# Optimization experiments

Measured on AMD Instinct MI355X. Metric: run time of the kernel, lower is better.

The kernel has to match this reference:

```python
import jax, jax.numpy as jnp
import numpy as np

N_NODES = 20000
N_EDGES = 100000
NODE_IN = 16
EDGE_IN = 10
LEAK = 0.1
EPS = 1e-5


def setup_inputs() -> dict:
    key = jax.random.key(0)
    ks = iter(jax.random.split(key, 40))

    def rn(shape, scale):
        return jax.random.normal(next(ks), shape, dtype=jnp.float32) * scale

    inp = {}
    inp["x"] = jax.random.normal(next(ks), (N_NODES, NODE_IN), dtype=jnp.float32)
    inp["e"] = jax.random.normal(next(ks), (N_EDGES, EDGE_IN), dtype=jnp.float32)
    inp["edge_index"] = jax.random.randint(next(ks), (2, N_EDGES), 0, N_NODES, dtype=jnp.int64)
    inp["xbatch"] = jnp.zeros((N_NODES,), dtype=jnp.int64)

    # BatchNorm affine params
    inp["bn_node_g"] = jnp.ones((NODE_IN,), jnp.float32)
    inp["bn_node_b"] = jnp.zeros((NODE_IN,), jnp.float32)
    inp["bn_edge_g"] = jnp.ones((EDGE_IN,), jnp.float32)
    inp["bn_edge_b"] = jnp.zeros((EDGE_IN,), jnp.float32)

    # nn1: Lin(10,16) -> LeakyReLU -> Lin(16, 16*32) -> LeakyReLU
    inp["nn1_w1"] = rn((EDGE_IN, 16), 0.3); inp["nn1_b1"] = jnp.zeros((16,), jnp.float32)
    inp["nn1_w2"] = rn((16, 16 * 32), 0.25); inp["nn1_b2"] = jnp.zeros((16 * 32,), jnp.float32)
    # nn2: Lin(10,32) -> LeakyReLU -> Lin(32, 32*64) -> LeakyReLU
    inp["nn2_w1"] = rn((EDGE_IN, 32), 0.3); inp["nn2_b1"] = jnp.zeros((32,), jnp.float32)
    inp["nn2_w2"] = rn((32, 32 * 64), 0.18); inp["nn2_b2"] = jnp.zeros((32 * 64,), jnp.float32)

    # NNConv root weights + biases
    inp["l1_root"] = rn((16, 32), 0.25); inp["l1_bias"] = jnp.zeros((32,), jnp.float32)
    inp["l2_root"] = rn((32, 64), 0.18); inp["l2_bias"] = jnp.zeros((64,), jnp.float32)

    # edge_pred_mlp: 138 -> 64 -> 32 -> 16 -> 8 -> 2
    dims = [2 * 64 + EDGE_IN, 64, 32, 16, 8, 2]
    for i in range(5):
        inp[f"mlp_w{i+1}"] = rn((dims[i], dims[i + 1]), 1.0 / np.sqrt(dims[i]))
        inp[f"mlp_b{i+1}"] = jnp.zeros((dims[i + 1],), jnp.float32)
    return inp


def _bn(v, g, b):
    # BatchNorm1d, training-mode batch statistics (biased variance), eps=1e-5
    m = v.mean(axis=0)
    var = v.var(axis=0)
    return (v - m) * jax.lax.rsqrt(var + EPS) * g + b


def _lrelu(v):
    return jax.nn.leaky_relu(v, LEAK)


def _nnconv(x, src, dst, e, w1, b1, w2, b2, root, bias, c_in, c_out):
    # edge MLP -> per-edge weight matrix [E, c_in, c_out]
    h = _lrelu(e @ w1 + b1)
    W = _lrelu(h @ w2 + b2).reshape(-1, c_in, c_out)
    # gather source features, per-edge matmul, scatter-add to targets
    msg = jnp.einsum("ei,eio->eo", x[src], W)
    agg = jax.ops.segment_sum(msg, dst, num_segments=x.shape[0])
    return agg + x @ root + bias


def reference(x, e, edge_index, xbatch,
              bn_node_g, bn_node_b, bn_edge_g, bn_edge_b,
              nn1_w1, nn1_b1, nn1_w2, nn1_b2,
              nn2_w1, nn2_b1, nn2_w2, nn2_b2,
              l1_root, l1_bias, l2_root, l2_bias,
              mlp_w1, mlp_b1, mlp_w2, mlp_b2, mlp_w3, mlp_b3,
              mlp_w4, mlp_b4, mlp_w5, mlp_b5):
    src, dst = edge_index[0], edge_index[1]
    e = _bn(e, bn_edge_g, bn_edge_b)
    x = _bn(x, bn_node_g, bn_node_b)
    x = _nnconv(x, src, dst, e, nn1_w1, nn1_b1, nn1_w2, nn1_b2, l1_root, l1_bias, 16, 32)
    x = _nnconv(x, src, dst, e, nn2_w1, nn2_b1, nn2_w2, nn2_b2, l2_root, l2_bias, 32, 64)
    # MetaLayer edge model: cat(source, target, edge_attr) -> MLP -> [E, 2]
    h = jnp.concatenate([x[src], x[dst], e], axis=1)
    h = _lrelu(h @ mlp_w1 + mlp_b1)
    h = _lrelu(h @ mlp_w2 + mlp_b2)
    h = _lrelu(h @ mlp_w3 + mlp_b3)
    h = _lrelu(h @ mlp_w4 + mlp_b4)
    edge_pred = h @ mlp_w5 + mlp_b5
    return edge_pred
```

## Files before the change

### kernel.cpp

```cpp
#include <hip/hip_runtime.h>
#include <cstdint>

#define N_NODES 20000
#define N_EDGES 100000
#define BN_EPS 1e-5f

typedef __attribute__((ext_vector_type(8))) short short8;
typedef __attribute__((ext_vector_type(4))) float floatx4;

__device__ __forceinline__ float lrelu(float v) { return fmaxf(v, 0.1f * v); }
__device__ __forceinline__ float4 ld4(const float* p) { return *reinterpret_cast<const float4*>(p); }
__device__ __forceinline__ float2 ld2(const float* p) { return *reinterpret_cast<const float2*>(p); }

__device__ __forceinline__ void atomAddF(float* p, float v) {
#if defined(__HIP_DEVICE_COMPILE__)
    unsafeAtomicAdd(p, v);
#else
    atomicAdd(p, v);
#endif
}

__device__ __forceinline__ unsigned short f2bf(float f) {
    union { float f; uint32_t u; } v; v.f = f;
    uint32_t r = v.u + 0x7fffu + ((v.u >> 16) & 1u);
    return (unsigned short)(r >> 16);
}
__device__ __forceinline__ uint32_t pack2(float a, float b) {
    return (uint32_t)f2bf(a) | ((uint32_t)f2bf(b) << 16);
}
__device__ __forceinline__ short8 pack8(float4 a, float4 b) {
    union { short8 s; uint32_t u[4]; } r;
    r.u[0] = pack2(a.x, a.y); r.u[1] = pack2(a.z, a.w);
    r.u[2] = pack2(b.x, b.y); r.u[3] = pack2(b.z, b.w);
    return r.s;
}

__device__ void stats10_dev(const float* __restrict__ v, int rows, float* __restrict__ out,
                            int blk, int nblk, float* sh) {
    if (threadIdx.x < 20) sh[threadIdx.x] = 0.f;
    __syncthreads();
    int nf2 = rows * 5;
    int stride = nblk * 256;
    int g = blk * 256 + threadIdx.x;
    int c2 = g % 5;
    float s0 = 0.f, s1 = 0.f, q0 = 0.f, q1 = 0.f;
    const float2* p = reinterpret_cast<const float2*>(v);
    for (int i = g; i < nf2; i += stride) {
        float2 t = p[i];
        s0 += t.x; s1 += t.y; q0 += t.x * t.x; q1 += t.y * t.y;
    }
    atomicAdd(&sh[2 * c2], s0);
    atomicAdd(&sh[2 * c2 + 1], s1);
    atomicAdd(&sh[10 + 2 * c2], q0);
    atomicAdd(&sh[10 + 2 * c2 + 1], q1);
    __syncthreads();
    if (threadIdx.x < 20) atomAddF(&out[threadIdx.x], sh[threadIdx.x]);
}

__device__ void stats16_dev(const float* __restrict__ v, int rows, float* __restrict__ out,
                            int blk, int nblk, float* sh) {
    if (threadIdx.x < 32) sh[threadIdx.x] = 0.f;
    __syncthreads();
    int nf4 = rows * 4;
    int stride = nblk * 256;
    int g = blk * 256 + threadIdx.x;
    int cg = (g & 3) * 4;
    float s[4] = {0.f, 0.f, 0.f, 0.f}, q[4] = {0.f, 0.f, 0.f, 0.f};
    const float4* p = reinterpret_cast<const float4*>(v);
    for (int i = g; i < nf4; i += stride) {
        float4 t = p[i];
        s[0] += t.x; s[1] += t.y; s[2] += t.z; s[3] += t.w;
        q[0] += t.x * t.x; q[1] += t.y * t.y; q[2] += t.z * t.z; q[3] += t.w * t.w;
    }
    #pragma unroll
    for (int off = 32; off >= 4; off >>= 1) {
        #pragma unroll
        for (int j = 0; j < 4; ++j) {
            s[j] += __shfl_down(s[j], off, 64);
            q[j] += __shfl_down(q[j], off, 64);
        }
    }
    if ((threadIdx.x & 63) < 4) {
        #pragma unroll
        for (int j = 0; j < 4; ++j) {
            atomicAdd(&sh[cg + j], s[j]);
            atomicAdd(&sh[16 + cg + j], q[j]);
        }
    }
    __syncthreads();
    if (threadIdx.x < 32) atomAddF(&out[threadIdx.x], sh[threadIdx.x]);
}

template<int CIN, int COUT, int H, int OCH>
__device__ void convpack_row(const float* __restrict__ w2, const float* __restrict__ b2,
                             char* __restrict__ pk, int r) {
    constexpr int NROW = CIN * OCH;
    constexpr int WB = NROW * 64;
    constexpr int PACKB = WB + NROW * 4;
    if (r >= CIN * COUT) return;
    int chunk = r / NROW;
    int rem = r % NROW;
    int i = rem / OCH, ol = rem % OCH;
    int n = i * COUT + chunk * OCH + ol;
    char* base = pk + (size_t)chunk * PACKB;
    uint32_t pkv[16];
    #pragma unroll
    for (int t = 0; t < 16; ++t) pkv[t] = 0;
    #pragma unroll
    for (int k = 0; k < H; k += 2)
        pkv[k >> 1] = pack2(w2[(size_t)k * (CIN * COUT) + n],
                            w2[(size_t)(k + 1) * (CIN * COUT) + n]);
    uint4* ob = reinterpret_cast<uint4*>(base);
    #pragma unroll
    for (int q = 0; q < 4; ++q)
        ob[(size_t)q * NROW + rem] = make_uint4(pkv[4 * q], pkv[4 * q + 1],
                                                pkv[4 * q + 2], pkv[4 * q + 3]);
    ((float*)(base + WB))[rem] = b2[n];
}

#define P1_S10 120
#define P1_S16 120
__global__ __launch_bounds__(256)
void prep1_kernel(const float* __restrict__ e, const float* __restrict__ x,
                  float* __restrict__ stats_e, float* __restrict__ stats_x,
                  const int* __restrict__ dst, int* __restrict__ counts,
                  const float* __restrict__ nn1_w2, const float* __restrict__ nn1_b2, char* __restrict__ cpack1,
                  const float* __restrict__ nn2_w2, const float* __restrict__ nn2_b2, char* __restrict__ cpack2,
                  const float* __restrict__ mw1, unsigned short* __restrict__ w1t,
                  const float* __restrict__ mw2, const float* __restrict__ mb2,
                  const float* __restrict__ mw3, const float* __restrict__ mb3,
                  const float* __restrict__ mw4, const float* __restrict__ mb4,
                  const float* __restrict__ mw5, const float* __restrict__ mb5,
                  float* __restrict__ mlpw)
{
    __shared__ float sh[32];
    int b = blockIdx.x;
    if (b < P1_S10) {
        stats10_dev(e, N_EDGES, stats_e, b, P1_S10, sh);
    } else if (b < P1_S10 + P1_S16) {
        stats16_dev(x, N_NODES, stats_x, b - P1_S10, P1_S16, sh);
    } else if (b < 631) {
        int i = (b - 240) * 256 + threadIdx.x;
        if (i < N_EDGES) atomicAdd(&counts[dst[i]], 1);
    } else if (b < 633) {
        convpack_row<16, 32, 16, 32>(nn1_w2, nn1_b2, cpack1, (b - 631) * 256 + threadIdx.x);
    } else if (b < 641) {
        convpack_row<32, 64, 32, 16>(nn2_w2, nn2_b2, cpack2, (b - 633) * 256 + threadIdx.x);
    } else {
        if (threadIdx.x < 64) {
            int o = threadIdx.x;
            for (int k = 0; k < 160; k += 2) {
                float a = (k < 138) ? mw1[(size_t)k * 64 + o] : 0.f;
                float c = (k + 1 < 138) ? mw1[(size_t)(k + 1) * 64 + o] : 0.f;
                *reinterpret_cast<uint32_t*>(w1t + (size_t)o * 160 + k) = pack2(a, c);
            }
        }
        for (int i = threadIdx.x; i < 2764; i += 256) {
            float v = 0.f;
            if (i < 2048) v = mw2[i];
            else if (i < 2560) v = mw3[i - 2048];
            else if (i < 2688) v = mw4[i - 2560];
            else if (i < 2704) v = mw5[i - 2688];
            else if (i < 2736) v = mb2[i - 2704];
            else if (i < 2752) v = mb3[i - 2736];
            else if (i < 2760) v = mb4[i - 2752];
            else if (i < 2762) v = mb5[i - 2760];
            mlpw[i] = v;
        }
    }
}

__global__ void scan_kernel(const int* __restrict__ counts, int* __restrict__ starts,
                            int* __restrict__ cursor, int n) {
    __shared__ int part[256];
    const int CH = (n + 255) / 256;
    int t = threadIdx.x;
    int lo = t * CH, hi = min(lo + CH, n);
    int s = 0;
    for (int i = lo; i < hi; ++i) s += counts[i];
    part[t] = s;
    __syncthreads();
    if (t == 0) {
        int acc = 0;
        for (int i = 0; i < 256; ++i) { int v = part[i]; part[i] = acc; acc += v; }
    }
    __syncthreads();
    int acc = part[t];
    for (int i = lo; i < hi; ++i) {
        starts[i] = acc; cursor[i] = acc; acc += counts[i];
    }
}

#define P2_N16 1250
#define P2_SCAT 391
#define P2_HGEN 391
__global__ __launch_bounds__(256)
void prep2_kernel(const float* __restrict__ x, const float* __restrict__ stats_x,
                  const float* __restrict__ bn_node_g, const float* __restrict__ bn_node_b,
                  float* __restrict__ x_n,
                  const int* __restrict__ dst, int* __restrict__ cursor, int* __restrict__ elist,
                  const float* __restrict__ e, const float* __restrict__ stats_e,
                  const float* __restrict__ bn_edge_g, const float* __restrict__ bn_edge_b,
                  float* __restrict__ e_n,
                  const float* __restrict__ w1a, const float* __restrict__ b1a,
                  const float* __restrict__ w1b, const float* __restrict__ b1b,
                  unsigned short* __restrict__ h1, unsigned short* __restrict__ h2)
{
    int b = blockIdx.x;
    if (b < P2_N16) {
        int idx = b * 256 + threadIdx.x;
        if (idx >= N_NODES * 16) return;
        int c = idx & 15;
        float N = (float)N_NODES;
        float m = stats_x[c] / N;
        float var = stats_x[16 + c] / N - m * m;
        float sc = rsqrtf(var + BN_EPS) * bn_node_g[c];
        x_n[idx] = (x[idx] - m) * sc + bn_node_b[c];
    } else if (b < P2_N16 + P2_SCAT) {
        int i = (b - P2_N16) * 256 + threadIdx.x;
        if (i < N_EDGES) {
            int p = atomicAdd(&cursor[dst[i]], 1);
            elist[p] = i;
        }
    } else {
        int eg = (b - P2_N16 - P2_SCAT) * 256 + threadIdx.x;
        if (eg >= N_EDGES) return;
        float ev[10];
        float Ecnt = (float)N_EDGES;
        #pragma unroll
        for (int j = 0; j < 10; ++j) {
            float m = stats_e[j] / Ecnt;
            float var = stats_e[10 + j] / Ecnt - m * m;
            float sc = rsqrtf(var + BN_EPS) * bn_edge_g[j];
            ev[j] = (e[(size_t)eg * 10 + j] - m) * sc + bn_edge_b[j];
            e_n[(size_t)eg * 10 + j] = ev[j];
        }
        {
            uint32_t pk[16];
            #pragma unroll
            for (int t = 0; t < 16; ++t) pk[t] = 0;
            #pragma unroll
            for (int k = 0; k < 16; k += 2) {
                float a0 = b1a[k], a1 = b1a[k + 1];
                #pragma unroll
                for (int j = 0; j < 10; ++j) {
                    a0 += ev[j] * w1a[j * 16 + k];
                    a1 += ev[j] * w1a[j * 16 + k + 1];
                }
                pk[k >> 1] = pack2(lrelu(a0), lrelu(a1));
            }
            uint4* o = reinterpret_cast<uint4*>(h1 + (size_t)eg * 32);
            o[0] = make_uint4(pk[0], pk[1], pk[2], pk[3]);
            o[1] = make_uint4(pk[4], pk[5], pk[6], pk[7]);
            o[2] = make_uint4(pk[8], pk[9], pk[10], pk[11]);
            o[3] = make_uint4(pk[12], pk[13], pk[14], pk[15]);
        }
        {
            uint32_t pk[16];
            #pragma unroll
            for (int k = 0; k < 32; k += 2) {
                float a0 = b1b[k], a1 = b1b[k + 1];
                #pragma unroll
                for (int j = 0; j < 10; ++j) {
                    a0 += ev[j] * w1b[j * 32 + k];
                    a1 += ev[j] * w1b[j * 32 + k + 1];
                }
                pk[k >> 1] = pack2(lrelu(a0), lrelu(a1));
            }
            uint4* o = reinterpret_cast<uint4*>(h2 + (size_t)eg * 32);
            o[0] = make_uint4(pk[0], pk[1], pk[2], pk[3]);
            o[1] = make_uint4(pk[4], pk[5], pk[6], pk[7]);
            o[2] = make_uint4(pk[8], pk[9], pk[10], pk[11]);
            o[3] = make_uint4(pk[12], pk[13], pk[14], pk[15]);
        }
    }
}

template<int CIN, int COUT, int OCH, int NE>
__global__ __launch_bounds__(256, 4)
void conv_lds_kernel(const unsigned short* __restrict__ hbuf,
                     const char* __restrict__ pack,
                     const int* __restrict__ src,
                     const float* __restrict__ xin,
                     float* __restrict__ msgbuf,
                     int n_edges)
{
    constexpr int NCH = COUT / OCH;
    constexpr int NROW = CIN * OCH;
    constexpr int WB = NROW * 64;
    constexpr int PACKB = WB + NROW * 4;
    __shared__ char smem[PACKB];

    int tid = threadIdx.x;
    int chunk = blockIdx.x % NCH;
    int eblk = blockIdx.x / NCH;

    {
        const uint4* g = reinterpret_cast<const uint4*>(pack + (size_t)chunk * PACKB);
        uint4* s = reinterpret_cast<uint4*>(smem);
        #pragma unroll 1
        for (int o = tid; o < PACKB / 16; o += 256) s[o] = g[o];
    }
    __syncthreads();

    int wv = tid >> 6, lane = tid & 63;
    int el = lane & 15, quad = lane >> 4;
    int g0 = (eblk * 4 + wv) * NE;

    const unsigned short* wlds = reinterpret_cast<const unsigned short*>(smem)
                                 + ((size_t)quad * NROW + el) * 8;
    const float* blds = reinterpret_cast<const float*>(smem + WB) + quad * 4;

    #pragma unroll 1
    for (int gI = 0; gI < NE; ++gI) {
        int e0 = (g0 + gI) * 16;
        if (e0 >= n_edges) return;
        int e = e0 + el;
        int s = src[e];

        short8 bfrag = *reinterpret_cast<const short8*>(hbuf + (size_t)e * 32 + quad * 8);

        float xr[CIN];
        #pragma unroll
        for (int i = 0; i < CIN; i += 4) {
            float4 v = ld4(xin + (size_t)s * CIN + i);
            xr[i] = v.x; xr[i + 1] = v.y; xr[i + 2] = v.z; xr[i + 3] = v.w;
        }

        floatx4 msg[OCH / 16];
        #pragma unroll
        for (int t = 0; t < OCH / 16; ++t) msg[t] = (floatx4){0.f, 0.f, 0.f, 0.f};

        #pragma unroll 8
        for (int i = 0; i < CIN; ++i) {
            float xi = xr[i];
            #pragma unroll
            for (int ot = 0; ot < OCH / 16; ++ot) {
                short8 af = *reinterpret_cast<const short8*>(wlds + (i * OCH + ot * 16) * 8);
                float4 bb = *reinterpret_cast<const float4*>(blds + i * OCH + ot * 16);
                floatx4 c = {bb.x, bb.y, bb.z, bb.w};
                c = __builtin_amdgcn_mfma_f32_16x16x32_bf16(af, bfrag, c, 0, 0, 0);
                #pragma unroll
                for (int r = 0; r < 4; ++r)
                    msg[ot][r] += xi * lrelu(c[r]);
            }
        }

        float* orow = msgbuf + (size_t)e * COUT + chunk * OCH;
        #pragma unroll
        for (int ot = 0; ot < OCH / 16; ++ot)
            *reinterpret_cast<float4*>(orow + ot * 16 + quad * 4) =
                make_float4(msg[ot][0], msg[ot][1], msg[ot][2], msg[ot][3]);
    }
}

template<int CIN, int C>
__global__ __launch_bounds__(256)
void gather_root_kernel(const float* __restrict__ xin, const float* __restrict__ w,
                        const float* __restrict__ bias,
                        const float* __restrict__ msg,
                        const int* __restrict__ starts, const int* __restrict__ counts,
                        const int* __restrict__ elist,
                        float* __restrict__ xout, int nodes)
{
    constexpr int NPW = 64 / C;
    int wv = blockIdx.x * 4 + (threadIdx.x >> 6);
    int lane = threadIdx.x & 63;
    int node = wv * NPW + lane / C;
    int ch = lane % C;
    if (node >= nodes) return;
    float acc = bias[ch];
    const float* xrow = xin + (size_t)node * CIN;
    #pragma unroll
    for (int i = 0; i < CIN; ++i) acc += xrow[i] * w[i * C + ch];
    int s0 = starts[node], cnt = counts[node];
    int i = 0;
    for (; i + 3 < cnt; i += 4) {
        int ea = elist[s0 + i], eb = elist[s0 + i + 1];
        int ec = elist[s0 + i + 2], ed = elist[s0 + i + 3];
        float m0 = msg[(size_t)ea * C + ch];
        float m1 = msg[(size_t)eb * C + ch];
        float m2 = msg[(size_t)ec * C + ch];
        float m3 = msg[(size_t)ed * C + ch];
        acc += (m0 + m1) + (m2 + m3);
    }
    for (; i < cnt; ++i) acc += msg[(size_t)elist[s0 + i] * C + ch];
    xout[(size_t)node * C + ch] = acc;
}

__global__ __launch_bounds__(256)
void mlp2_kernel(const float* __restrict__ x2, const float* __restrict__ e_n,
                 const int* __restrict__ src, const int* __restrict__ dst,
                 const unsigned short* __restrict__ w1t, const float* __restrict__ b1,
                 const float* __restrict__ mlpw,
                 float* __restrict__ out, int n_edges)
{
    __shared__ float wl[2764];
    __shared__ float a1t[4 * 1092];
    __shared__ float a2scr[4 * 528];

    int tid = threadIdx.x;
    {
        const uint4* g = reinterpret_cast<const uint4*>(mlpw);
        uint4* s = reinterpret_cast<uint4*>(wl);
        #pragma unroll 1
        for (int i = tid; i < 691; i += 256) s[i] = g[i];
    }

    int wv = tid >> 6, lane = tid & 63;
    int el = lane & 15, quad = lane >> 4;
    int e = blockIdx.x * 64 + wv * 16 + el;
    int eS = (e < n_edges) ? e : (n_edges - 1);
    int sN = src[eS], dN = dst[eS];

    short8 bf[5];
    {
        const float* rs = x2 + (size_t)sN * 64 + quad * 8;
        const float* rd = x2 + (size_t)dN * 64 + quad * 8;
        bf[0] = pack8(ld4(rs), ld4(rs + 4));
        bf[1] = pack8(ld4(rs + 32), ld4(rs + 36));
        bf[2] = pack8(ld4(rd), ld4(rd + 4));
        bf[3] = pack8(ld4(rd + 32), ld4(rd + 36));
        union { short8 s; uint32_t u[4]; } t;
        t.u[0] = t.u[1] = t.u[2] = t.u[3] = 0;
        const float* ep = e_n + (size_t)eS * 10;
        if (quad == 0) {
            float2 p0 = ld2(ep), p1 = ld2(ep + 2), p2 = ld2(ep + 4), p3 = ld2(ep + 6);
            t.u[0] = pack2(p0.x, p0.y); t.u[1] = pack2(p1.x, p1.y);
            t.u[2] = pack2(p2.x, p2.y); t.u[3] = pack2(p3.x, p3.y);
        } else if (quad == 1) {
            float2 p4 = ld2(ep + 8);
            t.u[0] = pack2(p4.x, p4.y);
        }
        bf[4] = t.s;
    }

    float* slab = &a1t[wv * 1092];
    {
        floatx4 acc[4];
        #pragma unroll
        for (int ot = 0; ot < 4; ++ot) {
            float4 bb = ld4(b1 + ot * 16 + quad * 4);
            acc[ot] = (floatx4){bb.x, bb.y, bb.z, bb.w};
        }
        #pragma unroll
        for (int ks = 0; ks < 5; ++ks) {
            #pragma unroll
            for (int ot = 0; ot < 4; ++ot) {
                short8 af = *reinterpret_cast<const short8*>(
                    w1t + (size_t)(ot * 16 + el) * 160 + ks * 32 + quad * 8);
                acc[ot] = __builtin_amdgcn_mfma_f32_16x16x32_bf16(af, bf[ks], acc[ot], 0, 0, 0);
            }
        }
        #pragma unroll
        for (int ot = 0; ot < 4; ++ot) {
            #pragma unroll
            for (int r = 0; r < 4; ++r)
                slab[(ot * 16 + quad * 4 + r) * 17 + el] = lrelu(acc[ot][r]);
        }
    }
    __syncthreads();

    const float* w2l = wl;            const float* w3l = wl + 2048;
    const float* w4l = wl + 2560;     const float* w5l = wl + 2688;
    const float* b2l = wl + 2704;     const float* b3l = wl + 2736;
    const float* b4l = wl + 2752;     const float* b5l = wl + 2760;
    float* a2s = &a2scr[wv * 528];
    float* a3s = slab;
    float* a4s = slab + 512;
    int p = quad;

    {
        float a2[8];
        #pragma unroll
        for (int j = 0; j < 8; ++j) a2[j] = b2l[p * 8 + j];
        #pragma unroll 4
        for (int i = 0; i < 64; ++i) {
            float ai = slab[i * 17 + el];
            #pragma unroll
            for (int j = 0; j < 8; ++j) a2[j] += ai * w2l[i * 32 + p * 8 + j];
        }
        #pragma unroll
        for (int j = 0; j < 8; ++j) a2s[el * 33 + p * 8 + j] = lrelu(a2[j]);
    }
    {
        float a3[4];
        #pragma unroll
        for (int j = 0; j < 4; ++j) a3[j] = b3l[p * 4 + j];
        #pragma unroll 4
        for (int i = 0; i < 32; ++i) {
            float ai = a2s[el * 33 + i];
            #pragma unroll
            for (int j = 0; j < 4; ++j) a3[j] += ai * w3l[i * 16 + p * 4 + j];
        }
        #pragma unroll
        for (int j = 0; j < 4; ++j) a3s[el * 17 + p * 4 + j] = lrelu(a3[j]);
    }
    {
        float a4[2];
        a4[0] = b4l[p * 2]; a4[1] = b4l[p * 2 + 1];
        #pragma unroll
        for (int i = 0; i < 16; ++i) {
            float ai = a3s[el * 17 + i];
            a4[0] += ai * w4l[i * 8 + p * 2];
            a4[1] += ai * w4l[i * 8 + p * 2 + 1];
        }
        a4s[el * 9 + p * 2]     = lrelu(a4[0]);
        a4s[el * 9 + p * 2 + 1] = lrelu(a4[1]);
    }
    if (p < 2) {
        float o = b5l[p];
        #pragma unroll
        for (int i = 0; i < 8; ++i) o += a4s[el * 9 + i] * w5l[i * 2 + p];
        if (e < n_edges) out[(size_t)e * 2 + p] = o;
    }
}

extern "C" void kernel_launch(void* const* d_in, const int* in_sizes, int n_in,
                              void* d_out, int out_size, void* d_ws, size_t ws_size,
                              hipStream_t stream)
{
    const float* x  = (const float*)d_in[0];
    const float* e  = (const float*)d_in[1];
    const int*   ei = (const int*)d_in[2];
    const float* bn_node_g = (const float*)d_in[4];
    const float* bn_node_b = (const float*)d_in[5];
    const float* bn_edge_g = (const float*)d_in[6];
    const float* bn_edge_b = (const float*)d_in[7];
    const float* nn1_w1 = (const float*)d_in[8];
    const float* nn1_b1 = (const float*)d_in[9];
    const float* nn1_w2 = (const float*)d_in[10];
    const float* nn1_b2 = (const float*)d_in[11];
    const float* nn2_w1 = (const float*)d_in[12];
    const float* nn2_b1 = (const float*)d_in[13];
    const float* nn2_w2 = (const float*)d_in[14];
    const float* nn2_b2 = (const float*)d_in[15];
    const float* l1_root = (const float*)d_in[16];
    const float* l1_bias = (const float*)d_in[17];
    const float* l2_root = (const float*)d_in[18];
    const float* l2_bias = (const float*)d_in[19];
    const float* mw1 = (const float*)d_in[20]; const float* mb1 = (const float*)d_in[21];
    const float* mw2 = (const float*)d_in[22]; const float* mb2 = (const float*)d_in[23];
    const float* mw3 = (const float*)d_in[24]; const float* mb3 = (const float*)d_in[25];
    const float* mw4 = (const float*)d_in[26]; const float* mb4 = (const float*)d_in[27];
    const float* mw5 = (const float*)d_in[28]; const float* mb5 = (const float*)d_in[29];

    const int* src = ei;
    const int* dst = ei + N_EDGES;

    float* ws = (float*)d_ws;
    float* stats_e = ws;
    float* stats_x = ws + 32;
    int* counts = (int*)(ws + 64);
    int* starts = counts + 20000;
    int* cursor = starts + 20000;
    int* elist  = cursor + 20000;
    float* e_n = ws + 64 + 160000;
    float* x_n = e_n + 1000000;
    float* x1  = x_n + 320000;
    float* x2  = x1 + 640000;
    float* msg = x2 + 1280000;
    unsigned short* h1   = (unsigned short*)(msg + 6400000);
    unsigned short* h2   = h1 + 3200000;
    unsigned short* w1t  = h2 + 3200000;
    char* cpack1 = (char*)(w1t + 10240);
    char* cpack2 = cpack1 + 34816;
    float* mlpw = (float*)(cpack2 + 4 * 34816);
    float* out = (float*)d_out;

    (void)hipMemsetAsync(d_ws, 0, (64 + 20000) * 4, stream);

    prep1_kernel<<<642, 256, 0, stream>>>(
        e, x, stats_e, stats_x, dst, counts,
        nn1_w2, nn1_b2, cpack1, nn2_w2, nn2_b2, cpack2,
        mw1, w1t, mw2, mb2, mw3, mb3, mw4, mb4, mw5, mb5, mlpw);

    scan_kernel<<<1, 256, 0, stream>>>(counts, starts, cursor, N_NODES);

    prep2_kernel<<<P2_N16 + P2_SCAT + P2_HGEN, 256, 0, stream>>>(
        x, stats_x, bn_node_g, bn_node_b, x_n,
        dst, cursor, elist,
        e, stats_e, bn_edge_g, bn_edge_b, e_n,
        nn1_w1, nn1_b1, nn2_w1, nn2_b1, h1, h2);

    const int NGRP = (N_EDGES + 15) / 16;
    const int CB = (NGRP + 8 - 1) / 8;

    conv_lds_kernel<16, 32, 32, 2><<<CB, 256, 0, stream>>>(h1, cpack1, src, x_n, msg, N_EDGES);
    gather_root_kernel<16, 32><<<(N_NODES / 2 + 3) / 4, 256, 0, stream>>>(
        x_n, l1_root, l1_bias, msg, starts, counts, elist, x1, N_NODES);

    conv_lds_kernel<32, 64, 16, 2><<<CB * 4, 256, 0, stream>>>(h2, cpack2, src, x1, msg, N_EDGES);
    gather_root_kernel<32, 64><<<(N_NODES + 3) / 4, 256, 0, stream>>>(
        x1, l2_root, l2_bias, msg, starts, counts, elist, x2, N_NODES);

    mlp2_kernel<<<(N_EDGES + 63) / 64, 256, 0, stream>>>(
        x2, e_n, src, dst, w1t, mb1, mlpw, out, N_EDGES);
}
```

Measured before the change: 336.5 us.

## Vectorize lrelu/accumulate as packed float2, warp-scan prefix, larger conv blocks

Recasts the per-MFMA LeakyReLU and x-weighted accumulation as float2 vector operations so the compiler can emit packed FP32 math (v_pk_mul/v_pk_fma). Replaces the serial single-thread prefix over 256 partials in the scan kernel with a wavefront shuffle scan plus a per-wave offset. Doubles the edge groups each conv block handles (NE 2→4) and halves the grid, amortizing the LDS weight-pack load over more work at the cost of fewer blocks in flight.

```diff
diff --git a/kernel.cpp b/kernel.cpp
--- a/kernel.cpp
+++ b/kernel.cpp
@@ -7,6 +7,7 @@
 
 typedef __attribute__((ext_vector_type(8))) short short8;
 typedef __attribute__((ext_vector_type(4))) float floatx4;
+typedef __attribute__((ext_vector_type(2))) float float2v;
 
 __device__ __forceinline__ float lrelu(float v) { return fmaxf(v, 0.1f * v); }
 __device__ __forceinline__ float4 ld4(const float* p) { return *reinterpret_cast<const float4*>(p); }
@@ -172,20 +173,24 @@
 
 __global__ void scan_kernel(const int* __restrict__ counts, int* __restrict__ starts,
                             int* __restrict__ cursor, int n) {
-    __shared__ int part[256];
+    __shared__ int wsum[4];
     const int CH = (n + 255) / 256;
     int t = threadIdx.x;
+    int lane = t & 63, wv = t >> 6;
     int lo = t * CH, hi = min(lo + CH, n);
     int s = 0;
     for (int i = lo; i < hi; ++i) s += counts[i];
-    part[t] = s;
+    int v = s;
+    #pragma unroll
+    for (int off = 1; off < 64; off <<= 1) {
+        int u = __shfl_up(v, off, 64);
+        if (lane >= off) v += u;
+    }
+    if (lane == 63) wsum[wv] = v;
     __syncthreads();
-    if (t == 0) {
-        int acc = 0;
-        for (int i = 0; i < 256; ++i) { int v = part[i]; part[i] = acc; acc += v; }
-    }
-    __syncthreads();
-    int acc = part[t];
+    int woff = 0;
+    for (int w = 0; w < wv; ++w) woff += wsum[w];
+    int acc = woff + v - s;
     for (int i = lo; i < hi; ++i) {
         starts[i] = acc; cursor[i] = acc; acc += counts[i];
     }
@@ -311,6 +316,8 @@
                                  + ((size_t)quad * NROW + el) * 8;
     const float* blds = reinterpret_cast<const float*>(smem + WB) + quad * 4;
 
+    const float2v pt = {0.1f, 0.1f};
+
     #pragma unroll 1
     for (int gI = 0; gI < NE; ++gI) {
         int e0 = (g0 + gI) * 16;
@@ -327,22 +334,28 @@
             xr[i] = v.x; xr[i + 1] = v.y; xr[i + 2] = v.z; xr[i + 3] = v.w;
         }
 
-        floatx4 msg[OCH / 16];
-        #pragma unroll
-        for (int t = 0; t < OCH / 16; ++t) msg[t] = (floatx4){0.f, 0.f, 0.f, 0.f};
+        float2v msg0[OCH / 16], msg1[OCH / 16];
+        #pragma unroll
+        for (int t = 0; t < OCH / 16; ++t) {
+            msg0[t] = (float2v){0.f, 0.f};
+            msg1[t] = (float2v){0.f, 0.f};
+        }
 
         #pragma unroll 8
         for (int i = 0; i < CIN; ++i) {
-            float xi = xr[i];
+            float2v xi2 = {xr[i], xr[i]};
             #pragma unroll
             for (int ot = 0; ot < OCH / 16; ++ot) {
                 short8 af = *reinterpret_cast<const short8*>(wlds + (i * OCH + ot * 16) * 8);
                 float4 bb = *reinterpret_cast<const float4*>(blds + i * OCH + ot * 16);
                 floatx4 c = {bb.x, bb.y, bb.z, bb.w};
                 c = __builtin_amdgcn_mfma_f32_16x16x32_bf16(af, bfrag, c, 0, 0, 0);
-                #pragma unroll
-                for (int r = 0; r < 4; ++r)
-                    msg[ot][r] += xi * lrelu(c[r]);
+                float2v c0 = {c[0], c[1]};
+                float2v c1 = {c[2], c[3]};
+                float2v m0 = __builtin_elementwise_max(c0, c0 * pt);
+                float2v m1 = __builtin_elementwise_max(c1, c1 * pt);
+                msg0[ot] += xi2 * m0;
+                msg1[ot] += xi2 * m1;
             }
         }
 
@@ -350,7 +363,7 @@
         #pragma unroll
         for (int ot = 0; ot < OCH / 16; ++ot)
             *reinterpret_cast<float4*>(orow + ot * 16 + quad * 4) =
-                make_float4(msg[ot][0], msg[ot][1], msg[ot][2], msg[ot][3]);
+                make_float4(msg0[ot][0], msg0[ot][1], msg1[ot][0], msg1[ot][1]);
     }
 }
 
@@ -584,13 +597,13 @@
         nn1_w1, nn1_b1, nn2_w1, nn2_b1, h1, h2);
 
     const int NGRP = (N_EDGES + 15) / 16;
-    const int CB = (NGRP + 8 - 1) / 8;
-
-    conv_lds_kernel<16, 32, 32, 2><<<CB, 256, 0, stream>>>(h1, cpack1, src, x_n, msg, N_EDGES);
+    const int CB = (NGRP + 15) / 16;
+
+    conv_lds_kernel<16, 32, 32, 4><<<CB, 256, 0, stream>>>(h1, cpack1, src, x_n, msg, N_EDGES);
     gather_root_kernel<16, 32><<<(N_NODES / 2 + 3) / 4, 256, 0, stream>>>(
         x_n, l1_root, l1_bias, msg, starts, counts, elist, x1, N_NODES);
 
-    conv_lds_kernel<32, 64, 16, 2><<<CB * 4, 256, 0, stream>>>(h2, cpack2, src, x1, msg, N_EDGES);
+    conv_lds_kernel<32, 64, 16, 4><<<CB * 4, 256, 0, stream>>>(h2, cpack2, src, x1, msg, N_EDGES);
     gather_root_kernel<32, 64><<<(N_NODES + 3) / 4, 256, 0, stream>>>(
         x1, l2_root, l2_bias, msg, starts, counts, elist, x2, N_NODES);
 
```

Result: no change. 339.9 us (+1.0%).
